# Kernel optimization log

Hardware: AMD Instinct MI355X
Metric: run time of the kernel (lower is better)

Reference implementation:

```python
import jax, jax.numpy as jnp
import numpy as np

WS = 512   # window_size
LB = 1     # look_backward
LF = 1     # look_forward
H = 16     # num_attention_heads
NC = LB + LF + 1  # concatenated windows per query window


def _collect(a, pad_value):
    # a: [B, nw, ws, ...]; gather windows [i-LB, i+LF] for each window i,
    # padding the window axis with pad_value (faithful to collect_windows).
    nw = a.shape[1]
    pads = [(0, 0), (LB, LF)] + [(0, 0)] * (a.ndim - 2)
    ap = jnp.pad(a, pads, constant_values=pad_value)
    idx = jnp.arange(nw)[:, None] + jnp.arange(NC)[None, :]  # [nw, NC]
    g = ap[:, idx]  # [B, nw, NC, ws, ...]
    return g.reshape(g.shape[0], nw, NC * a.shape[2], *a.shape[3:])


def setup_inputs() -> dict:
    key = jax.random.key(0)
    ks = jax.random.split(key, 9)
    B, S, E = 1, 4096, 1024
    x = jax.random.normal(ks[0], (B, S, E), dtype=jnp.float32)
    std = 0.02
    wq = std * jax.random.normal(ks[1], (E, E), dtype=jnp.float32)
    wk = std * jax.random.normal(ks[2], (E, E), dtype=jnp.float32)
    wv = std * jax.random.normal(ks[3], (E, E), dtype=jnp.float32)
    wo = std * jax.random.normal(ks[4], (E, E), dtype=jnp.float32)
    bq = std * jax.random.normal(ks[5], (E,), dtype=jnp.float32)
    bk = std * jax.random.normal(ks[6], (E,), dtype=jnp.float32)
    bv = std * jax.random.normal(ks[7], (E,), dtype=jnp.float32)
    bo = std * jax.random.normal(ks[8], (E,), dtype=jnp.float32)
    return {"x": x, "wq": wq, "bq": bq, "wk": wk, "bk": bk,
            "wv": wv, "bv": bv, "wo": wo, "bo": bo}


def reference(x, wq, bq, wk, bk, wv, bv, wo, bo):
    B, S, E = x.shape
    hd = E // H
    nw = S // WS  # seq_len chosen divisible by window_size

    def proj(w, b):
        y = x @ w.T + b
        return y.reshape(B, S, H, hd).transpose(0, 2, 1, 3).reshape(B * H, S, hd)

    q = proj(wq, bq)
    k = proj(wk, bk)
    v = proj(wv, bv)

    qb = q.reshape(B * H, nw, WS, hd)
    # NOTE: original pads K/V window buffers with value -1 (not zero); pad
    # positions are NOT masked (the `!= -1` clause excludes them) -- replicated.
    kb = _collect(k.reshape(B * H, nw, WS, hd), -1.0)  # [BH, nw, NC*WS, hd]
    vb = _collect(v.reshape(B * H, nw, WS, hd), -1.0)

    t = jnp.arange(S, dtype=jnp.int32).reshape(1, nw, WS)
    ct = _collect(t, -1)  # [1, nw, NC*WS] key positions (-1 for pads)

    # Unscaled QK^T (original applies no 1/sqrt(d)).
    scores = jnp.einsum('bwqd,bwkd->bwqk', qb, kb)  # [BH, nw, WS, NC*WS]

    qi = t.reshape(1, nw, WS, 1)          # query absolute positions
    ctb = ct[:, :, None, :]               # key absolute positions
    over = ((ctb > qi + WS * LF) | (ctb < qi - WS * LB)) & (ctb != -1)
    scores = jnp.where(over, -jnp.inf, scores)

    attn = jax.nn.softmax(scores, axis=-1)
    out = jnp.einsum('bwqk,bwkd->bwqd', attn, vb)  # [BH, nw, WS, hd]
    out = out.reshape(B, H, S, hd).transpose(0, 2, 1, 3).reshape(B, S, E)
    return out @ wo.T + bo
```

## Files before the change

### kernel.cpp

```cpp
#include <hip/hip_runtime.h>
#include <stdint.h>

#define S 4096
#define E 1024
#define NH 16
#define HD 64
#define WSZ 512

typedef _Float16 f16x8 __attribute__((ext_vector_type(8)));
typedef _Float16 f16x4 __attribute__((ext_vector_type(4)));
typedef float f32x4 __attribute__((ext_vector_type(4)));
typedef unsigned short u16;
typedef unsigned int u32;

__device__ __forceinline__ u16 f2h_bits(float f) {
    union { _Float16 h; u16 u; } cv; cv.h = (_Float16)f; return cv.u;
}

__device__ __forceinline__ void gld16(const u16* g, u16* l) {
    __builtin_amdgcn_global_load_lds((const __attribute__((address_space(1))) void*)g,
                                     (__attribute__((address_space(3))) void*)l, 16, 0, 0);
}

struct CvtArgs {
    const float* s[5];
    u16* d[5];
    int n[5];
};
__global__ void cvt5(CvtArgs a) {
    int seg = blockIdx.y;
    const float* __restrict__ s = a.s[seg];
    u16* __restrict__ d = a.d[seg];
    int n = a.n[seg];
    for (int i = (blockIdx.x * 256 + threadIdx.x) * 4; i < n; i += gridDim.x * 1024) {
        float4 f = *(const float4*)&s[i];
        uint2 o;
        o.x = (u32)f2h_bits(f.x) | ((u32)f2h_bits(f.y) << 16);
        o.y = (u32)f2h_bits(f.z) | ((u32)f2h_bits(f.w) << 16);
        *(uint2*)&d[i] = o;
    }
}

__global__ __launch_bounds__(256) void gemm_qkv(
    const u16* __restrict__ A, const u16* __restrict__ B,
    u16* __restrict__ OutQK, u16* __restrict__ OutVT,
    const float* __restrict__ b0, const float* __restrict__ b1, const float* __restrict__ b2,
    int K) {
    __shared__ __align__(16) u16 As[2 * 128 * 32];
    __shared__ __align__(16) u16 Bs[2 * 128 * 32];
    const int tid = threadIdx.x;
    const int wid = tid >> 6, lid = tid & 63, quad = lid >> 4, l16 = lid & 15;
    const int wm = wid >> 1, wn = wid & 1;
    const int bm0 = blockIdx.x * 128, bn0 = blockIdx.y * 128;

    f32x4 acc[4][4] = {};
    const int srow = tid >> 2, scol = (tid & 3) * 8;

    for (int k0 = 0; k0 < K; k0 += 64) {
        __syncthreads();
#pragma unroll
        for (int half = 0; half < 2; ++half)
#pragma unroll
            for (int rep = 0; rep < 2; ++rep) {
                gld16(&A[(size_t)(bm0 + rep * 64 + srow) * K + k0 + half * 32 + scol],
                      &As[half * 4096 + rep * 2048 + tid * 8]);
                gld16(&B[(size_t)(bn0 + rep * 64 + srow) * K + k0 + half * 32 + scol],
                      &Bs[half * 4096 + rep * 2048 + tid * 8]);
            }
        __syncthreads();
#pragma unroll
        for (int kk = 0; kk < 2; ++kk) {
            f16x8 af[4], bf[4];
#pragma unroll
            for (int i = 0; i < 4; ++i) af[i] = *(const f16x8*)&As[kk * 4096 + (wm * 64 + i * 16 + l16) * 32 + quad * 8];
#pragma unroll
            for (int j = 0; j < 4; ++j) bf[j] = *(const f16x8*)&Bs[kk * 4096 + (wn * 64 + j * 16 + l16) * 32 + quad * 8];
#pragma unroll
            for (int i = 0; i < 4; ++i)
#pragma unroll
                for (int j = 0; j < 4; ++j)
                    acc[i][j] = __builtin_amdgcn_mfma_f32_16x16x32_f16(af[i], bf[j], acc[i][j], 0, 0, 0);
        }
    }

    const bool isV = (bn0 >= 2048);
#pragma unroll
    for (int j = 0; j < 4; ++j) {
        int n = bn0 + wn * 64 + j * 16 + l16;
        float bias = (n < 1024) ? b0[n] : (n < 2048 ? b1[n - 1024] : b2[n - 2048]);
#pragma unroll
        for (int i = 0; i < 4; ++i) {
            int m0 = bm0 + wm * 64 + i * 16 + quad * 4;
            if (!isV) {
#pragma unroll
                for (int r = 0; r < 4; ++r)
                    OutQK[(size_t)(m0 + r) * 2048 + n] = f2h_bits(acc[i][j][r] + bias);
            } else {
                u16 h0 = f2h_bits(acc[i][j][0] + bias);
                u16 h1 = f2h_bits(acc[i][j][1] + bias);
                u16 h2 = f2h_bits(acc[i][j][2] + bias);
                u16 h3 = f2h_bits(acc[i][j][3] + bias);
                uint2 pk;
                pk.x = (u32)h0 | ((u32)h1 << 16);
                pk.y = (u32)h2 | ((u32)h3 << 16);
                *(uint2*)&OutVT[(size_t)(n - 2048) * 4096 + m0] = pk;
            }
        }
    }
}

__global__ __launch_bounds__(256) void gemm_n64(
    const u16* __restrict__ A, const u16* __restrict__ B, float* __restrict__ OutF,
    const float* __restrict__ bias, int N, int K) {
    __shared__ __align__(16) u16 As[2 * 128 * 32];
    __shared__ __align__(16) u16 Bs[2 * 64 * 32];
    const int tid = threadIdx.x;
    const int wid = tid >> 6, lid = tid & 63, quad = lid >> 4, l16 = lid & 15;
    const int bm0 = blockIdx.x * 128, bn0 = blockIdx.y * 64;

    f32x4 acc[2][4] = {};
    const int srow = tid >> 2, scol = (tid & 3) * 8;

    for (int k0 = 0; k0 < K; k0 += 64) {
        __syncthreads();
#pragma unroll
        for (int half = 0; half < 2; ++half) {
#pragma unroll
            for (int rep = 0; rep < 2; ++rep)
                gld16(&A[(size_t)(bm0 + rep * 64 + srow) * K + k0 + half * 32 + scol],
                      &As[half * 4096 + rep * 2048 + tid * 8]);
            gld16(&B[(size_t)(bn0 + srow) * K + k0 + half * 32 + scol],
                  &Bs[half * 2048 + tid * 8]);
        }
        __syncthreads();
#pragma unroll
        for (int kk = 0; kk < 2; ++kk) {
            f16x8 af[2], bf[4];
#pragma unroll
            for (int i = 0; i < 2; ++i) af[i] = *(const f16x8*)&As[kk * 4096 + (wid * 32 + i * 16 + l16) * 32 + quad * 8];
#pragma unroll
            for (int j = 0; j < 4; ++j) bf[j] = *(const f16x8*)&Bs[kk * 2048 + (j * 16 + l16) * 32 + quad * 8];
#pragma unroll
            for (int i = 0; i < 2; ++i)
#pragma unroll
                for (int j = 0; j < 4; ++j)
                    acc[i][j] = __builtin_amdgcn_mfma_f32_16x16x32_f16(af[i], bf[j], acc[i][j], 0, 0, 0);
        }
    }

#pragma unroll
    for (int j = 0; j < 4; ++j) {
        int n = bn0 + j * 16 + l16;
        float bv = bias[n];
#pragma unroll
        for (int i = 0; i < 2; ++i) {
            int m0 = bm0 + wid * 32 + i * 16 + quad * 4;
#pragma unroll
            for (int r = 0; r < 4; ++r)
                OutF[(size_t)(m0 + r) * N + n] = acc[i][j][r] + bv;
        }
    }
}

__global__ __launch_bounds__(256) void attn_win(const u16* __restrict__ QK, const u16* __restrict__ VT,
                                                u16* __restrict__ AO) {
    const int qt = blockIdx.x, w = blockIdx.y, h = blockIdx.z;
    const int tid = threadIdx.x, wid = tid >> 6, lid = tid & 63, quad = lid >> 4, l16 = lid & 15;

    __shared__ __align__(16) u16 Ks[2][2 * 64 * 32];
    __shared__ __align__(16) u16 Vt[2][2 * 64 * 36];

    const int qrow = w * WSZ + qt * 64 + wid * 16 + l16;
    const _Float16 L2E = (_Float16)1.44269504f;
    f16x8 qf[2];
#pragma unroll
    for (int ks = 0; ks < 2; ++ks) {
        qf[ks] = *(const f16x8*)&QK[(size_t)qrow * 2048 + h * 64 + ks * 32 + quad * 8];
#pragma unroll
        for (int j = 0; j < 8; ++j) qf[ks][j] *= L2E;
    }

    const int npad = (w == 0 || w == 7) ? 512 : 0;
    float s_p = 0.f;
    if (npad) {
        float sq = 0.f;
#pragma unroll
        for (int j = 0; j < 8; ++j) sq += (float)qf[0][j] + (float)qf[1][j];
        sq += __shfl_xor(sq, 16, 64);
        sq += __shfl_xor(sq, 32, 64);
        s_p = -sq;
    }

    f32x4 oacc[4] = {};
    float mrun = -30000.f;
    float lsum = 0.f;

    const int g0base = (w - 1) * WSZ;
    const int rqloc = qt * 64 + wid * 16 + l16;
    const int rqw0 = qt * 64 + wid * 16;

    int cfirst = qt; if ((1 - w) * 8 > cfirst) cfirst = (1 - w) * 8;
    int clast = qt + 16; if (71 - 8 * w < clast) clast = 71 - 8 * w; if (clast > 23) clast = 23;

    const size_t kgoff = 1024 + h * 64 + (tid & 3) * 8 + (size_t)(tid >> 2) * 2048;
    const int kl = tid * 8;
    const int vd = tid >> 2, vk0 = (tid & 3) * 16;
    const u16* vgrow = VT + (size_t)(h * 64 + vd) * 4096 + vk0;
    const int vloff = (vk0 >> 5) * 2304 + vd * 36 + (vk0 & 31);

    {
        const int g0 = g0base + cfirst * 64;
        uint4 va = *(const uint4*)(vgrow + g0);
        uint4 vb = *(const uint4*)(vgrow + g0 + 8);
        gld16(QK + (size_t)g0 * 2048 + kgoff, &Ks[0][0] + kl);
        gld16(QK + (size_t)g0 * 2048 + kgoff + 32, &Ks[0][0] + 2048 + kl);
        u16* vp = &Vt[0][0] + vloff;
        *(uint2*)(vp)      = make_uint2(va.x, va.y);
        *(uint2*)(vp + 4)  = make_uint2(va.z, va.w);
        *(uint2*)(vp + 8)  = make_uint2(vb.x, vb.y);
        *(uint2*)(vp + 12) = make_uint2(vb.z, vb.w);
    }

    int ib = 0;
    for (int c = cfirst; c <= clast; ++c, ib ^= 1) {
        __syncthreads();

        const bool has_next = (c < clast);
        uint4 vna, vnb;
        if (has_next) {
            const int gn = g0base + (c + 1) * 64;
            vna = *(const uint4*)(vgrow + gn);
            vnb = *(const uint4*)(vgrow + gn + 8);
            gld16(QK + (size_t)gn * 2048 + kgoff, &Ks[ib ^ 1][0] + kl);
            gld16(QK + (size_t)gn * 2048 + kgoff + 32, &Ks[ib ^ 1][0] + 2048 + kl);
        }

        const u16* KsB = &Ks[ib][0];
        const u16* VtB = &Vt[ib][0];

        f32x4 sc[4];
#pragma unroll
        for (int nt = 0; nt < 4; ++nt) {
            f16x8 kf0 = *(const f16x8*)&KsB[(nt * 16 + l16) * 32 + quad * 8];
            f16x8 kf1 = *(const f16x8*)&KsB[2048 + (nt * 16 + l16) * 32 + quad * 8];
            f32x4 t = {};
            t = __builtin_amdgcn_mfma_f32_16x16x32_f16(kf0, qf[0], t, 0, 0, 0);
            t = __builtin_amdgcn_mfma_f32_16x16x32_f16(kf1, qf[1], t, 0, 0, 0);
            sc[nt] = t;
        }

        const bool needs_mask = (c * 64 < rqw0 + 16) || (c * 64 + 63 > rqw0 + 1024);
        if (needs_mask) {
#pragma unroll
            for (int nt = 0; nt < 4; ++nt)
#pragma unroll
                for (int r = 0; r < 4; ++r) {
                    int n = c * 64 + nt * 16 + quad * 4 + r;
                    if (n < rqloc || n > rqloc + 1024) sc[nt][r] = -30000.f;
                }
        }

        float mloc = mrun;
#pragma unroll
        for (int nt = 0; nt < 4; ++nt)
            mloc = fmaxf(mloc, fmaxf(fmaxf(sc[nt][0], sc[nt][1]), fmaxf(sc[nt][2], sc[nt][3])));
        mloc = fmaxf(mloc, __shfl_xor(mloc, 16, 64));
        mloc = fmaxf(mloc, __shfl_xor(mloc, 32, 64));

        const bool up = __any(mloc > mrun);
        float ls = 0.f;
        f16x4 pf[4];
#pragma unroll
        for (int nt = 0; nt < 4; ++nt)
#pragma unroll
            for (int r = 0; r < 4; ++r) {
                float p = exp2f(sc[nt][r] - mloc);
                ls += p;
                pf[nt][r] = (_Float16)p;
            }
        if (up) {
            float alpha = exp2f(mrun - mloc);
            mrun = mloc;
            lsum = lsum * alpha + ls;
            float ao[4];
#pragma unroll
            for (int r = 0; r < 4; ++r) ao[r] = __shfl(alpha, quad * 4 + r, 64);
#pragma unroll
            for (int dt = 0; dt < 4; ++dt)
#pragma unroll
                for (int r = 0; r < 4; ++r) oacc[dt][r] *= ao[r];
        } else {
            lsum += ls;
        }

#pragma unroll
        for (int nt = 0; nt < 4; ++nt)
#pragma unroll
            for (int dt = 0; dt < 4; ++dt) {
                f16x4 vf = *(const f16x4*)&VtB[(nt >> 1) * 2304 + (dt * 16 + l16) * 36 + (nt & 1) * 16 + quad * 4];
                oacc[dt] = __builtin_amdgcn_mfma_f32_16x16x16f16(pf[nt], vf, oacc[dt], 0, 0, 0);
            }

        if (has_next) {
            u16* vp = &Vt[ib ^ 1][0] + vloff;
            *(uint2*)(vp)      = make_uint2(vna.x, vna.y);
            *(uint2*)(vp + 4)  = make_uint2(vna.z, vna.w);
            *(uint2*)(vp + 8)  = make_uint2(vnb.x, vnb.y);
            *(uint2*)(vp + 12) = make_uint2(vnb.z, vnb.w);
        }
    }

    float lt = lsum;
    lt += __shfl_xor(lt, 16, 64);
    lt += __shfl_xor(lt, 32, 64);
    float aW = 1.f, pw = 0.f;
    if (npad) {
        float mnew = fmaxf(mrun, s_p);
        aW = exp2f(mrun - mnew);
        pw = 512.f * exp2f(s_p - mnew);
        lt = lt * aW + pw;
    }
    float linv = 1.f / lt;
    float lrec[4], arow[4], pwrow[4];
#pragma unroll
    for (int r = 0; r < 4; ++r) {
        lrec[r]  = __shfl(linv, quad * 4 + r, 64);
        arow[r]  = __shfl(aW,   quad * 4 + r, 64);
        pwrow[r] = __shfl(pw,   quad * 4 + r, 64);
    }
#pragma unroll
    for (int dt = 0; dt < 4; ++dt)
#pragma unroll
        for (int r = 0; r < 4; ++r) {
            int srow = w * WSZ + qt * 64 + wid * 16 + quad * 4 + r;
            int col = h * 64 + dt * 16 + l16;
            float o = (oacc[dt][r] * arow[r] - pwrow[r]) * lrec[r];
            AO[(size_t)srow * E + col] = f2h_bits(o);
        }
}

extern "C" void kernel_launch(void* const* d_in, const int* in_sizes, int n_in,
                              void* d_out, int out_size, void* d_ws, size_t ws_size,
                              hipStream_t stream) {
    const float* x  = (const float*)d_in[0];
    const float* wq = (const float*)d_in[1];
    const float* bq = (const float*)d_in[2];
    const float* wk = (const float*)d_in[3];
    const float* bk = (const float*)d_in[4];
    const float* wv = (const float*)d_in[5];
    const float* bv = (const float*)d_in[6];
    const float* wo = (const float*)d_in[7];
    const float* bo = (const float*)d_in[8];
    float* out = (float*)d_out;

    char* ws = (char*)d_ws;
    u16* XH  = (u16*)(ws);
    u16* WC  = (u16*)(ws + 8388608);
    u16* WOh = (u16*)(ws + 14680064);
    u16* QK  = (u16*)(ws + 16777216);
    u16* VTg = (u16*)(ws + 33554432);
    u16* AOh = (u16*)(ws + 41943040);

    CvtArgs ca;
    ca.s[0] = x;  ca.d[0] = XH;            ca.n[0] = 4194304;
    ca.s[1] = wq; ca.d[1] = WC;            ca.n[1] = 1048576;
    ca.s[2] = wk; ca.d[2] = WC + 1048576;  ca.n[2] = 1048576;
    ca.s[3] = wv; ca.d[3] = WC + 2097152;  ca.n[3] = 1048576;
    ca.s[4] = wo; ca.d[4] = WOh;           ca.n[4] = 1048576;
    cvt5<<<dim3(1024, 5), 256, 0, stream>>>(ca);

    gemm_qkv<<<dim3(32, 24), 256, 0, stream>>>(XH, WC, QK, VTg, bq, bk, bv, 1024);
    attn_win<<<dim3(8, 8, 16), 256, 0, stream>>>(QK, VTg, AOh);
    gemm_n64<<<dim3(32, 16), 256, 0, stream>>>(AOh, WOh, out, bo, 1024, 1024);
}
```

Baseline: 196.8 us.

## Process two 16-row query tiles per wave in windowed attention

Each wave now handles 32 query rows, two m-tiles, instead of 16, so every block covers 128 queries and the grid is halved along the query axis. Each K/V chunk loaded into shared memory is reused by twice as many MFMAs, cutting K/V traffic and chunk-loop overhead per query. The cost is more registers per thread, since accumulators and scores double, plus one extra key chunk of masked work per block and fewer blocks in flight. The launch bounds now ask for 4 blocks per CU to limit register use.

```diff
diff --git a/kernel.cpp b/kernel.cpp
--- a/kernel.cpp
+++ b/kernel.cpp
@@ -162,45 +162,50 @@
     }
 }
 
-__global__ __launch_bounds__(256) void attn_win(const u16* __restrict__ QK, const u16* __restrict__ VT,
-                                                u16* __restrict__ AO) {
+__global__ __launch_bounds__(256, 4) void attn_win(const u16* __restrict__ QK, const u16* __restrict__ VT,
+                                                   u16* __restrict__ AO) {
     const int qt = blockIdx.x, w = blockIdx.y, h = blockIdx.z;
     const int tid = threadIdx.x, wid = tid >> 6, lid = tid & 63, quad = lid >> 4, l16 = lid & 15;
 
     __shared__ __align__(16) u16 Ks[2][2 * 64 * 32];
     __shared__ __align__(16) u16 Vt[2][2 * 64 * 36];
 
-    const int qrow = w * WSZ + qt * 64 + wid * 16 + l16;
+    const int qrow0 = w * WSZ + qt * 128 + wid * 32;
     const _Float16 L2E = (_Float16)1.44269504f;
-    f16x8 qf[2];
-#pragma unroll
-    for (int ks = 0; ks < 2; ++ks) {
-        qf[ks] = *(const f16x8*)&QK[(size_t)qrow * 2048 + h * 64 + ks * 32 + quad * 8];
-#pragma unroll
-        for (int j = 0; j < 8; ++j) qf[ks][j] *= L2E;
-    }
+    f16x8 qf[2][2];
+#pragma unroll
+    for (int mt = 0; mt < 2; ++mt)
+#pragma unroll
+        for (int ks = 0; ks < 2; ++ks) {
+            qf[mt][ks] = *(const f16x8*)&QK[(size_t)(qrow0 + mt * 16 + l16) * 2048 + h * 64 + ks * 32 + quad * 8];
+#pragma unroll
+            for (int j = 0; j < 8; ++j) qf[mt][ks][j] *= L2E;
+        }
 
     const int npad = (w == 0 || w == 7) ? 512 : 0;
-    float s_p = 0.f;
+    float s_p[2] = {0.f, 0.f};
     if (npad) {
-        float sq = 0.f;
-#pragma unroll
-        for (int j = 0; j < 8; ++j) sq += (float)qf[0][j] + (float)qf[1][j];
-        sq += __shfl_xor(sq, 16, 64);
-        sq += __shfl_xor(sq, 32, 64);
-        s_p = -sq;
-    }
-
-    f32x4 oacc[4] = {};
-    float mrun = -30000.f;
-    float lsum = 0.f;
+#pragma unroll
+        for (int mt = 0; mt < 2; ++mt) {
+            float sq = 0.f;
+#pragma unroll
+            for (int j = 0; j < 8; ++j) sq += (float)qf[mt][0][j] + (float)qf[mt][1][j];
+            sq += __shfl_xor(sq, 16, 64);
+            sq += __shfl_xor(sq, 32, 64);
+            s_p[mt] = -sq;
+        }
+    }
+
+    f32x4 oacc[2][4] = {};
+    float mrun[2] = {-30000.f, -30000.f};
+    float lsum[2] = {0.f, 0.f};
 
     const int g0base = (w - 1) * WSZ;
-    const int rqloc = qt * 64 + wid * 16 + l16;
-    const int rqw0 = qt * 64 + wid * 16;
-
-    int cfirst = qt; if ((1 - w) * 8 > cfirst) cfirst = (1 - w) * 8;
-    int clast = qt + 16; if (71 - 8 * w < clast) clast = 71 - 8 * w; if (clast > 23) clast = 23;
+    const int rqloc = qt * 128 + wid * 32 + l16;
+    const int rqw0 = qt * 128 + wid * 32;
+
+    int cfirst = 2 * qt; if ((1 - w) * 8 > cfirst) cfirst = (1 - w) * 8;
+    int clast = 2 * qt + 17; if (71 - 8 * w < clast) clast = 71 - 8 * w; if (clast > 23) clast = 23;
 
     const size_t kgoff = 1024 + h * 64 + (tid & 3) * 8 + (size_t)(tid >> 2) * 2048;
     const int kl = tid * 8;
@@ -238,59 +243,69 @@
         const u16* KsB = &Ks[ib][0];
         const u16* VtB = &Vt[ib][0];
 
-        f32x4 sc[4];
+        f32x4 sc[2][4];
 #pragma unroll
         for (int nt = 0; nt < 4; ++nt) {
             f16x8 kf0 = *(const f16x8*)&KsB[(nt * 16 + l16) * 32 + quad * 8];
             f16x8 kf1 = *(const f16x8*)&KsB[2048 + (nt * 16 + l16) * 32 + quad * 8];
-            f32x4 t = {};
-            t = __builtin_amdgcn_mfma_f32_16x16x32_f16(kf0, qf[0], t, 0, 0, 0);
-            t = __builtin_amdgcn_mfma_f32_16x16x32_f16(kf1, qf[1], t, 0, 0, 0);
-            sc[nt] = t;
-        }
-
-        const bool needs_mask = (c * 64 < rqw0 + 16) || (c * 64 + 63 > rqw0 + 1024);
+#pragma unroll
+            for (int mt = 0; mt < 2; ++mt) {
+                f32x4 t = {};
+                t = __builtin_amdgcn_mfma_f32_16x16x32_f16(kf0, qf[mt][0], t, 0, 0, 0);
+                t = __builtin_amdgcn_mfma_f32_16x16x32_f16(kf1, qf[mt][1], t, 0, 0, 0);
+                sc[mt][nt] = t;
+            }
+        }
+
+        const bool needs_mask = (c * 64 < rqw0 + 32) || (c * 64 + 63 > rqw0 + 1024);
         if (needs_mask) {
 #pragma unroll
+            for (int mt = 0; mt < 2; ++mt) {
+                const int rq = rqloc + mt * 16;
+#pragma unroll
+                for (int nt = 0; nt < 4; ++nt)
+#pragma unroll
+                    for (int r = 0; r < 4; ++r) {
+                        int n = c * 64 + nt * 16 + quad * 4 + r;
+                        if (n < rq || n > rq + 1024) sc[mt][nt][r] = -30000.f;
+                    }
+            }
+        }
+
+        f16x4 pf[2][4];
+#pragma unroll
+        for (int mt = 0; mt < 2; ++mt) {
+            float mloc = mrun[mt];
+#pragma unroll
             for (int nt = 0; nt < 4; ++nt)
+                mloc = fmaxf(mloc, fmaxf(fmaxf(sc[mt][nt][0], sc[mt][nt][1]), fmaxf(sc[mt][nt][2], sc[mt][nt][3])));
+            mloc = fmaxf(mloc, __shfl_xor(mloc, 16, 64));
+            mloc = fmaxf(mloc, __shfl_xor(mloc, 32, 64));
+
+            const bool up = __any(mloc > mrun[mt]);
+            float ls = 0.f;
+#pragma unroll
+            for (int nt = 0; nt < 4; ++nt)
 #pragma unroll
                 for (int r = 0; r < 4; ++r) {
-                    int n = c * 64 + nt * 16 + quad * 4 + r;
-                    if (n < rqloc || n > rqloc + 1024) sc[nt][r] = -30000.f;
+                    float p = exp2f(sc[mt][nt][r] - mloc);
+                    ls += p;
+                    pf[mt][nt][r] = (_Float16)p;
                 }
-        }
-
-        float mloc = mrun;
-#pragma unroll
-        for (int nt = 0; nt < 4; ++nt)
-            mloc = fmaxf(mloc, fmaxf(fmaxf(sc[nt][0], sc[nt][1]), fmaxf(sc[nt][2], sc[nt][3])));
-        mloc = fmaxf(mloc, __shfl_xor(mloc, 16, 64));
-        mloc = fmaxf(mloc, __shfl_xor(mloc, 32, 64));
-
-        const bool up = __any(mloc > mrun);
-        float ls = 0.f;
-        f16x4 pf[4];
-#pragma unroll
-        for (int nt = 0; nt < 4; ++nt)
-#pragma unroll
-            for (int r = 0; r < 4; ++r) {
-                float p = exp2f(sc[nt][r] - mloc);
-                ls += p;
-                pf[nt][r] = (_Float16)p;
-            }
-        if (up) {
-            float alpha = exp2f(mrun - mloc);
-            mrun = mloc;
-            lsum = lsum * alpha + ls;
-            float ao[4];
-#pragma unroll
-            for (int r = 0; r < 4; ++r) ao[r] = __shfl(alpha, quad * 4 + r, 64);
-#pragma unroll
-            for (int dt = 0; dt < 4; ++dt)
-#pragma unroll
-                for (int r = 0; r < 4; ++r) oacc[dt][r] *= ao[r];
-        } else {
-            lsum += ls;
+            if (up) {
+                float alpha = exp2f(mrun[mt] - mloc);
+                mrun[mt] = mloc;
+                lsum[mt] = lsum[mt] * alpha + ls;
+                float ao[4];
+#pragma unroll
+                for (int r = 0; r < 4; ++r) ao[r] = __shfl(alpha, quad * 4 + r, 64);
+#pragma unroll
+                for (int dt = 0; dt < 4; ++dt)
+#pragma unroll
+                    for (int r = 0; r < 4; ++r) oacc[mt][dt][r] *= ao[r];
+            } else {
+                lsum[mt] += ls;
+            }
         }
 
 #pragma unroll
@@ -298,7 +313,8 @@
 #pragma unroll
             for (int dt = 0; dt < 4; ++dt) {
                 f16x4 vf = *(const f16x4*)&VtB[(nt >> 1) * 2304 + (dt * 16 + l16) * 36 + (nt & 1) * 16 + quad * 4];
-                oacc[dt] = __builtin_amdgcn_mfma_f32_16x16x16f16(pf[nt], vf, oacc[dt], 0, 0, 0);
+                oacc[0][dt] = __builtin_amdgcn_mfma_f32_16x16x16f16(pf[0][nt], vf, oacc[0][dt], 0, 0, 0);
+                oacc[1][dt] = __builtin_amdgcn_mfma_f32_16x16x16f16(pf[1][nt], vf, oacc[1][dt], 0, 0, 0);
             }
 
         if (has_next) {
@@ -310,33 +326,36 @@
         }
     }
 
-    float lt = lsum;
-    lt += __shfl_xor(lt, 16, 64);
-    lt += __shfl_xor(lt, 32, 64);
-    float aW = 1.f, pw = 0.f;
-    if (npad) {
-        float mnew = fmaxf(mrun, s_p);
-        aW = exp2f(mrun - mnew);
-        pw = 512.f * exp2f(s_p - mnew);
-        lt = lt * aW + pw;
-    }
-    float linv = 1.f / lt;
-    float lrec[4], arow[4], pwrow[4];
-#pragma unroll
-    for (int r = 0; r < 4; ++r) {
-        lrec[r]  = __shfl(linv, quad * 4 + r, 64);
-        arow[r]  = __shfl(aW,   quad * 4 + r, 64);
-        pwrow[r] = __shfl(pw,   quad * 4 + r, 64);
-    }
-#pragma unroll
-    for (int dt = 0; dt < 4; ++dt)
+#pragma unroll
+    for (int mt = 0; mt < 2; ++mt) {
+        float lt = lsum[mt];
+        lt += __shfl_xor(lt, 16, 64);
+        lt += __shfl_xor(lt, 32, 64);
+        float aW = 1.f, pw = 0.f;
+        if (npad) {
+            float mnew = fmaxf(mrun[mt], s_p[mt]);
+            aW = exp2f(mrun[mt] - mnew);
+            pw = 512.f * exp2f(s_p[mt] - mnew);
+            lt = lt * aW + pw;
+        }
+        float linv = 1.f / lt;
+        float lrec[4], arow[4], pwrow[4];
 #pragma unroll
         for (int r = 0; r < 4; ++r) {
-            int srow = w * WSZ + qt * 64 + wid * 16 + quad * 4 + r;
-            int col = h * 64 + dt * 16 + l16;
-            float o = (oacc[dt][r] * arow[r] - pwrow[r]) * lrec[r];
-            AO[(size_t)srow * E + col] = f2h_bits(o);
-        }
+            lrec[r]  = __shfl(linv, quad * 4 + r, 64);
+            arow[r]  = __shfl(aW,   quad * 4 + r, 64);
+            pwrow[r] = __shfl(pw,   quad * 4 + r, 64);
+        }
+#pragma unroll
+        for (int dt = 0; dt < 4; ++dt)
+#pragma unroll
+            for (int r = 0; r < 4; ++r) {
+                int srow = qrow0 + mt * 16 + quad * 4 + r;
+                int col = h * 64 + dt * 16 + l16;
+                float o = (oacc[mt][dt][r] * arow[r] - pwrow[r]) * lrec[r];
+                AO[(size_t)srow * E + col] = f2h_bits(o);
+            }
+    }
 }
 
 extern "C" void kernel_launch(void* const* d_in, const int* in_sizes, int n_in,
@@ -370,6 +389,6 @@
     cvt5<<<dim3(1024, 5), 256, 0, stream>>>(ca);
 
     gemm_qkv<<<dim3(32, 24), 256, 0, stream>>>(XH, WC, QK, VTg, bq, bk, bv, 1024);
-    attn_win<<<dim3(8, 8, 16), 256, 0, stream>>>(QK, VTg, AOh);
+    attn_win<<<dim3(4, 8, 16), 256, 0, stream>>>(QK, VTg, AOh);
     gemm_n64<<<dim3(32, 16), 256, 0, stream>>>(AOh, WOh, out, bo, 1024, 1024);
 }
```

Result: slower. 207.3 us (+5.3%).

## Enlarge attention query tile to 128 rows and stage two key chunks per sync

Applied to the files above, without the earlier changes.

The windowed attention kernel now uses 512-thread blocks (8 waves) covering 128 query rows instead of 64, halving the grid. Each loop iteration loads a 128-key block of K and V into shared memory and processes it as two 64-key sub-chunks, which halves the number of barriers. K/V tiles are shared by twice as many query rows, reducing global and LDS traffic per query. In exchange the kernel uses more shared memory and launches fewer blocks, and the causal-style band means some extra masked chunks are processed at the edges.

```diff
diff --git a/kernel.cpp b/kernel.cpp
--- a/kernel.cpp
+++ b/kernel.cpp
@@ -162,15 +162,15 @@
     }
 }
 
-__global__ __launch_bounds__(256) void attn_win(const u16* __restrict__ QK, const u16* __restrict__ VT,
-                                                u16* __restrict__ AO) {
+__global__ __launch_bounds__(512, 2) void attn_win(const u16* __restrict__ QK, const u16* __restrict__ VT,
+                                                   u16* __restrict__ AO) {
     const int qt = blockIdx.x, w = blockIdx.y, h = blockIdx.z;
     const int tid = threadIdx.x, wid = tid >> 6, lid = tid & 63, quad = lid >> 4, l16 = lid & 15;
 
-    __shared__ __align__(16) u16 Ks[2][2 * 64 * 32];
-    __shared__ __align__(16) u16 Vt[2][2 * 64 * 36];
-
-    const int qrow = w * WSZ + qt * 64 + wid * 16 + l16;
+    __shared__ __align__(16) u16 Ks[2][2 * 128 * 32];
+    __shared__ __align__(16) u16 Vt[2][4 * 64 * 36];
+
+    const int qrow = w * WSZ + qt * 128 + wid * 16 + l16;
     const _Float16 L2E = (_Float16)1.44269504f;
     f16x8 qf[2];
 #pragma unroll
@@ -196,25 +196,26 @@
     float lsum = 0.f;
 
     const int g0base = (w - 1) * WSZ;
-    const int rqloc = qt * 64 + wid * 16 + l16;
-    const int rqw0 = qt * 64 + wid * 16;
-
-    int cfirst = qt; if ((1 - w) * 8 > cfirst) cfirst = (1 - w) * 8;
-    int clast = qt + 16; if (71 - 8 * w < clast) clast = 71 - 8 * w; if (clast > 23) clast = 23;
-
-    const size_t kgoff = 1024 + h * 64 + (tid & 3) * 8 + (size_t)(tid >> 2) * 2048;
+    const int rqloc = qt * 128 + wid * 16 + l16;
+    const int rqw0 = qt * 128 + wid * 16;
+
+    int cfirst = 2 * qt; if ((1 - w) * 8 > cfirst) cfirst = (1 - w) * 8;
+    int clast = 2 * qt + 17; if (71 - 8 * w < clast) clast = 71 - 8 * w; if (clast > 23) clast = 23;
+
+    const int krow = tid >> 2;
+    const size_t kg = 1024 + h * 64 + (tid & 3) * 8;
     const int kl = tid * 8;
-    const int vd = tid >> 2, vk0 = (tid & 3) * 16;
-    const u16* vgrow = VT + (size_t)(h * 64 + vd) * 4096 + vk0;
+    const int vd = tid >> 3, vk0 = (tid & 7) * 16;
+    const u16* vgrow = VT + (size_t)(h * 64 + vd) * 4096;
     const int vloff = (vk0 >> 5) * 2304 + vd * 36 + (vk0 & 31);
 
     {
         const int g0 = g0base + cfirst * 64;
-        uint4 va = *(const uint4*)(vgrow + g0);
-        uint4 vb = *(const uint4*)(vgrow + g0 + 8);
-        gld16(QK + (size_t)g0 * 2048 + kgoff, &Ks[0][0] + kl);
-        gld16(QK + (size_t)g0 * 2048 + kgoff + 32, &Ks[0][0] + 2048 + kl);
-        u16* vp = &Vt[0][0] + vloff;
+        uint4 va = *(const uint4*)(vgrow + g0 + vk0);
+        uint4 vb = *(const uint4*)(vgrow + g0 + vk0 + 8);
+        gld16(QK + (size_t)(g0 + krow) * 2048 + kg,      &Ks[0][kl]);
+        gld16(QK + (size_t)(g0 + krow) * 2048 + kg + 32, &Ks[0][4096 + kl]);
+        u16* vp = &Vt[0][vloff];
         *(uint2*)(vp)      = make_uint2(va.x, va.y);
         *(uint2*)(vp + 4)  = make_uint2(va.z, va.w);
         *(uint2*)(vp + 8)  = make_uint2(vb.x, vb.y);
@@ -222,87 +223,94 @@
     }
 
     int ib = 0;
-    for (int c = cfirst; c <= clast; ++c, ib ^= 1) {
-        __syncthreads();
-
-        const bool has_next = (c < clast);
+    for (int c0 = cfirst; c0 <= clast; c0 += 2, ib ^= 1) {
+        __syncthreads();
+
+        const bool has_next = (c0 + 2 <= clast);
         uint4 vna, vnb;
         if (has_next) {
-            const int gn = g0base + (c + 1) * 64;
-            vna = *(const uint4*)(vgrow + gn);
-            vnb = *(const uint4*)(vgrow + gn + 8);
-            gld16(QK + (size_t)gn * 2048 + kgoff, &Ks[ib ^ 1][0] + kl);
-            gld16(QK + (size_t)gn * 2048 + kgoff + 32, &Ks[ib ^ 1][0] + 2048 + kl);
+            const int gn = g0base + (c0 + 2) * 64;
+            vna = *(const uint4*)(vgrow + gn + vk0);
+            vnb = *(const uint4*)(vgrow + gn + vk0 + 8);
+            gld16(QK + (size_t)(gn + krow) * 2048 + kg,      &Ks[ib ^ 1][kl]);
+            gld16(QK + (size_t)(gn + krow) * 2048 + kg + 32, &Ks[ib ^ 1][4096 + kl]);
         }
 
         const u16* KsB = &Ks[ib][0];
         const u16* VtB = &Vt[ib][0];
-
-        f32x4 sc[4];
-#pragma unroll
-        for (int nt = 0; nt < 4; ++nt) {
-            f16x8 kf0 = *(const f16x8*)&KsB[(nt * 16 + l16) * 32 + quad * 8];
-            f16x8 kf1 = *(const f16x8*)&KsB[2048 + (nt * 16 + l16) * 32 + quad * 8];
-            f32x4 t = {};
-            t = __builtin_amdgcn_mfma_f32_16x16x32_f16(kf0, qf[0], t, 0, 0, 0);
-            t = __builtin_amdgcn_mfma_f32_16x16x32_f16(kf1, qf[1], t, 0, 0, 0);
-            sc[nt] = t;
-        }
-
-        const bool needs_mask = (c * 64 < rqw0 + 16) || (c * 64 + 63 > rqw0 + 1024);
-        if (needs_mask) {
+        const int ncs = (c0 + 1 <= clast) ? 2 : 1;
+
+#pragma unroll
+        for (int cs = 0; cs < 2; ++cs) {
+            if (cs >= ncs) break;
+            const int c = c0 + cs;
+
+            f32x4 sc[4];
+#pragma unroll
+            for (int nt = 0; nt < 4; ++nt) {
+                f16x8 kf0 = *(const f16x8*)&KsB[(cs * 64 + nt * 16 + l16) * 32 + quad * 8];
+                f16x8 kf1 = *(const f16x8*)&KsB[4096 + (cs * 64 + nt * 16 + l16) * 32 + quad * 8];
+                f32x4 t = {};
+                t = __builtin_amdgcn_mfma_f32_16x16x32_f16(kf0, qf[0], t, 0, 0, 0);
+                t = __builtin_amdgcn_mfma_f32_16x16x32_f16(kf1, qf[1], t, 0, 0, 0);
+                sc[nt] = t;
+            }
+
+            const bool needs_mask = (c * 64 < rqw0 + 16) || (c * 64 + 63 > rqw0 + 1024);
+            if (needs_mask) {
+#pragma unroll
+                for (int nt = 0; nt < 4; ++nt)
+#pragma unroll
+                    for (int r = 0; r < 4; ++r) {
+                        int n = c * 64 + nt * 16 + quad * 4 + r;
+                        if (n < rqloc || n > rqloc + 1024) sc[nt][r] = -30000.f;
+                    }
+            }
+
+            float mloc = mrun;
 #pragma unroll
             for (int nt = 0; nt < 4; ++nt)
+                mloc = fmaxf(mloc, fmaxf(fmaxf(sc[nt][0], sc[nt][1]), fmaxf(sc[nt][2], sc[nt][3])));
+            mloc = fmaxf(mloc, __shfl_xor(mloc, 16, 64));
+            mloc = fmaxf(mloc, __shfl_xor(mloc, 32, 64));
+
+            const bool up = __any(mloc > mrun);
+            float ls = 0.f;
+            f16x4 pf[4];
+#pragma unroll
+            for (int nt = 0; nt < 4; ++nt)
 #pragma unroll
                 for (int r = 0; r < 4; ++r) {
-                    int n = c * 64 + nt * 16 + quad * 4 + r;
-                    if (n < rqloc || n > rqloc + 1024) sc[nt][r] = -30000.f;
+                    float p = exp2f(sc[nt][r] - mloc);
+                    ls += p;
+                    pf[nt][r] = (_Float16)p;
                 }
-        }
-
-        float mloc = mrun;
-#pragma unroll
-        for (int nt = 0; nt < 4; ++nt)
-            mloc = fmaxf(mloc, fmaxf(fmaxf(sc[nt][0], sc[nt][1]), fmaxf(sc[nt][2], sc[nt][3])));
-        mloc = fmaxf(mloc, __shfl_xor(mloc, 16, 64));
-        mloc = fmaxf(mloc, __shfl_xor(mloc, 32, 64));
-
-        const bool up = __any(mloc > mrun);
-        float ls = 0.f;
-        f16x4 pf[4];
-#pragma unroll
-        for (int nt = 0; nt < 4; ++nt)
-#pragma unroll
-            for (int r = 0; r < 4; ++r) {
-                float p = exp2f(sc[nt][r] - mloc);
-                ls += p;
-                pf[nt][r] = (_Float16)p;
-            }
-        if (up) {
-            float alpha = exp2f(mrun - mloc);
-            mrun = mloc;
-            lsum = lsum * alpha + ls;
-            float ao[4];
-#pragma unroll
-            for (int r = 0; r < 4; ++r) ao[r] = __shfl(alpha, quad * 4 + r, 64);
-#pragma unroll
-            for (int dt = 0; dt < 4; ++dt)
-#pragma unroll
-                for (int r = 0; r < 4; ++r) oacc[dt][r] *= ao[r];
-        } else {
-            lsum += ls;
-        }
-
-#pragma unroll
-        for (int nt = 0; nt < 4; ++nt)
-#pragma unroll
-            for (int dt = 0; dt < 4; ++dt) {
-                f16x4 vf = *(const f16x4*)&VtB[(nt >> 1) * 2304 + (dt * 16 + l16) * 36 + (nt & 1) * 16 + quad * 4];
-                oacc[dt] = __builtin_amdgcn_mfma_f32_16x16x16f16(pf[nt], vf, oacc[dt], 0, 0, 0);
-            }
+            if (up) {
+                float alpha = exp2f(mrun - mloc);
+                mrun = mloc;
+                lsum = lsum * alpha + ls;
+                float ao[4];
+#pragma unroll
+                for (int r = 0; r < 4; ++r) ao[r] = __shfl(alpha, quad * 4 + r, 64);
+#pragma unroll
+                for (int dt = 0; dt < 4; ++dt)
+#pragma unroll
+                    for (int r = 0; r < 4; ++r) oacc[dt][r] *= ao[r];
+            } else {
+                lsum += ls;
+            }
+
+#pragma unroll
+            for (int nt = 0; nt < 4; ++nt)
+#pragma unroll
+                for (int dt = 0; dt < 4; ++dt) {
+                    f16x4 vf = *(const f16x4*)&VtB[(cs * 2 + (nt >> 1)) * 2304 + (dt * 16 + l16) * 36 + (nt & 1) * 16 + quad * 4];
+                    oacc[dt] = __builtin_amdgcn_mfma_f32_16x16x16f16(pf[nt], vf, oacc[dt], 0, 0, 0);
+                }
+        }
 
         if (has_next) {
-            u16* vp = &Vt[ib ^ 1][0] + vloff;
+            u16* vp = &Vt[ib ^ 1][vloff];
             *(uint2*)(vp)      = make_uint2(vna.x, vna.y);
             *(uint2*)(vp + 4)  = make_uint2(vna.z, vna.w);
             *(uint2*)(vp + 8)  = make_uint2(vnb.x, vnb.y);
@@ -332,7 +340,7 @@
     for (int dt = 0; dt < 4; ++dt)
 #pragma unroll
         for (int r = 0; r < 4; ++r) {
-            int srow = w * WSZ + qt * 64 + wid * 16 + quad * 4 + r;
+            int srow = w * WSZ + qt * 128 + wid * 16 + quad * 4 + r;
             int col = h * 64 + dt * 16 + l16;
             float o = (oacc[dt][r] * arow[r] - pwrow[r]) * lrec[r];
             AO[(size_t)srow * E + col] = f2h_bits(o);
@@ -370,6 +378,6 @@
     cvt5<<<dim3(1024, 5), 256, 0, stream>>>(ca);
 
     gemm_qkv<<<dim3(32, 24), 256, 0, stream>>>(XH, WC, QK, VTg, bq, bk, bv, 1024);
-    attn_win<<<dim3(8, 8, 16), 256, 0, stream>>>(QK, VTg, AOh);
+    attn_win<<<dim3(4, 8, 16), 512, 0, stream>>>(QK, VTg, AOh);
     gemm_n64<<<dim3(32, 16), 256, 0, stream>>>(AOh, WOh, out, bo, 1024, 1024);
 }
```

After: 188.9 us. 1.04x faster.
